# Kernel optimization log

Hardware: AMD Instinct MI355X
Metric: run time of the kernel (lower is better)

Reference implementation:

```python
import jax, jax.numpy as jnp
import numpy as np
from jax import lax

B, H, W, CIN = 4, 64, 64, 1024
CMID = 512
NA = 9  # 3 sizes * 3 ratios
PRE_NMS, POST_NMS, IOU_THR = 6000, 300, 0.7  # eval-mode caps (training=False)


def setup_inputs() -> dict:
    key = jax.random.key(0)
    ks = jax.random.split(key, 4)
    feats = jax.random.normal(ks[0], (B, H, W, CIN), jnp.float32)
    # anchors: normalized ccwh (cx, cy, w, h) on a stride-16 grid of a 1024px image
    stride, img = 16.0, 1024.0
    cx = (jnp.arange(W, dtype=jnp.float32) + 0.5) * stride / img
    cy = (jnp.arange(H, dtype=jnp.float32) + 0.5) * stride / img
    sizes = jnp.array([64.0, 128.0, 256.0])
    ratios = jnp.array([0.5, 1.0, 2.0])
    ws = (sizes[:, None] * jnp.sqrt(ratios)[None, :]).reshape(-1) / img  # [9]
    hs = (sizes[:, None] / jnp.sqrt(ratios)[None, :]).reshape(-1) / img  # [9]
    cyg, cxg = jnp.meshgrid(cy, cx, indexing='ij')  # [H,W]
    ancs = jnp.stack([
        jnp.broadcast_to(cxg[:, :, None], (H, W, NA)),
        jnp.broadcast_to(cyg[:, :, None], (H, W, NA)),
        jnp.broadcast_to(ws[None, None, :], (H, W, NA)),
        jnp.broadcast_to(hs[None, None, :], (H, W, NA)),
    ], axis=-1)
    ancs = jnp.broadcast_to(ancs[None], (B, H, W, NA, 4)).astype(jnp.float32)
    ancs_valid = jnp.ones((B, H, W, NA), jnp.float32)
    w_bneck = jax.random.normal(ks[1], (CIN, CMID), jnp.float32) * 0.01
    b_bneck = jnp.zeros((CMID,), jnp.float32)
    w_cls = jax.random.normal(ks[2], (CMID, NA), jnp.float32) * 0.01
    b_cls = jnp.zeros((NA,), jnp.float32)
    w_reg = jax.random.normal(ks[3], (CMID, NA * 4), jnp.float32) * 0.01
    b_reg = jnp.zeros((NA * 4,), jnp.float32)
    return dict(feats=feats, ancs=ancs, ancs_valid=ancs_valid,
                w_bneck=w_bneck, b_bneck=b_bneck, w_cls=w_cls, b_cls=b_cls,
                w_reg=w_reg, b_reg=b_reg)


def _nms(boxes, max_out, thr):
    # boxes [N,4] xyxy, sorted by score descending. Greedy NMS via lax.scan.
    x1, y1, x2, y2 = boxes[:, 0], boxes[:, 1], boxes[:, 2], boxes[:, 3]
    areas = (x2 - x1) * (y2 - y1)

    def step(valid, _):
        idx = jnp.argmax(valid)  # first still-valid box = highest score
        has = valid[idx]
        b = boxes[idx]
        a = areas[idx]
        iw = jnp.maximum(jnp.minimum(b[2], x2) - jnp.maximum(b[0], x1), 0.0)
        ih = jnp.maximum(jnp.minimum(b[3], y2) - jnp.maximum(b[1], y1), 0.0)
        inter = iw * ih
        union = a + areas - inter
        iou = jnp.where(union > 0, inter / union, 0.0)
        keep = valid & (iou <= thr)
        keep = keep.at[idx].set(False)
        return jnp.where(has, keep, valid), jnp.where(has, idx, -1)

    _, sel = lax.scan(step, jnp.ones(boxes.shape[0], bool), None, length=max_out)
    return sel  # [max_out] selected indices, -1 = no more boxes


def _forward(feats, ancs, w_bneck, b_bneck, w_cls, b_cls, w_reg, b_reg):
    h = jax.nn.relu(jnp.einsum('bhwc,cm->bhwm', feats, w_bneck) + b_bneck)
    cls_pred = jax.nn.sigmoid(jnp.einsum('bhwm,mo->bhwo', h, w_cls) + b_cls)
    reg_pred = (jnp.einsum('bhwm,mo->bhwo', h, w_reg) + b_reg).reshape(B, H, W, NA, 4)
    cls_f = cls_pred.reshape(-1)
    reg_f = reg_pred.reshape(-1, 4)
    anc_f = ancs.reshape(-1, 4)
    # apply_offsets in ccwh: cx += tx*w, cy += ty*h, w *= exp(tw), h *= exp(th)
    cx = anc_f[:, 0] + reg_f[:, 0] * anc_f[:, 2]
    cy = anc_f[:, 1] + reg_f[:, 1] * anc_f[:, 3]
    ww = anc_f[:, 2] * jnp.exp(reg_f[:, 2])
    hh = anc_f[:, 3] * jnp.exp(reg_f[:, 3])
    # ccwh -> xyxy, clip to [0,1]
    boxes = jnp.stack([cx - ww / 2, cy - hh / 2, cx + ww / 2, cy + hh / 2], axis=-1)
    boxes = jnp.clip(boxes, 0.0, 1.0)
    order = jnp.argsort(-cls_f)[:PRE_NMS]
    boxes = boxes[order]
    sel = _nms(boxes, POST_NMS, IOU_THR)
    # pad unselected slots with zeros (TF returns a variable-length tensor)
    proposals = jnp.where(sel[:, None] >= 0, boxes[jnp.clip(sel, 0)], 0.0)
    return cls_pred, reg_pred, proposals


def reference(feats, ancs, ancs_valid, w_bneck, b_bneck, w_cls, b_cls, w_reg, b_reg):
    # ancs_valid is reshaped but never used in the original extract_proposals
    return _forward(feats, ancs, w_bneck, b_bneck, w_cls, b_cls, w_reg, b_reg)
```

## Files before the change

kernel.cpp:

```cpp
#include <hip/hip_runtime.h>
#include <cstdint>
#include <cstddef>

#define P_TOT    16384
#define CIN      1024
#define CMID     512
#define NA       9
#define NANC     147456
#define PRE_NMS  6000
#define POST_NMS 300
#define IOU_THR  0.7f
#define NWORDS   94
#define NHCOPY   64

#define CLS_OFF  0
#define REG_OFF  147456
#define PROP_OFF 737280

#define WS_H        0u
#define WS_MASK     0u
#define WS_HISTN    8388608u
#define WS_LOGITS   33554432u
#define WS_BOXES    36700160u
#define WS_HIST     39059456u
#define WS_WCOMB    39059456u
#define WS_META     39321600u
#define WS_COLL     39321856u
#define WS_SBOX     39387392u
#define CAP_COLL    8192

__device__ __forceinline__ int imin(int a, int b) { return a < b ? a : b; }

__device__ __forceinline__ void gld_lds16(const float* g, float* l) {
    __builtin_amdgcn_global_load_lds(
        (const __attribute__((address_space(1))) void*)g,
        (__attribute__((address_space(3))) void*)l,
        16, 0, 0);
}

__global__ __launch_bounds__(256)
__attribute__((amdgpu_waves_per_eu(1, 2)))
void gemm1_kernel(
    const float* __restrict__ A, const float* __restrict__ Bw,
    const float* __restrict__ bias, float* __restrict__ C)
{
    __shared__ float As[2][16][132];
    __shared__ float Bs[2][16][128];

    const int t  = threadIdx.x;
    const int m0 = blockIdx.x * 128;
    const int n0 = blockIdx.y * 128;
    const int tx = t & 15;
    const int ty = t >> 4;

    const int ar0 = t >> 2;
    const int ac0 = (t & 3) * 4;

    const float* asrc0 = A + (size_t)(m0 + ar0) * CIN + ac0;
    const float* asrc1 = asrc0 + (size_t)64 * CIN;
    const float* bsrc  = Bw + (size_t)(t >> 5) * CMID + n0 + (t & 31) * 4;
    float* bdst0 = &Bs[0][0][0] + t * 4;
    float* bdst1 = &Bs[1][0][0] + t * 4;

    float4 c0a{0,0,0,0}, c0b{0,0,0,0}, c1a{0,0,0,0}, c1b{0,0,0,0};
    float4 c2a{0,0,0,0}, c2b{0,0,0,0}, c3a{0,0,0,0}, c3b{0,0,0,0};
    float4 c4a{0,0,0,0}, c4b{0,0,0,0}, c5a{0,0,0,0}, c5b{0,0,0,0};
    float4 c6a{0,0,0,0}, c6b{0,0,0,0}, c7a{0,0,0,0}, c7b{0,0,0,0};

    gld_lds16(bsrc, bdst0);
    gld_lds16(bsrc + 8 * CMID, bdst0 + 1024);
    float4 pa0 = *(const float4*)(asrc0);
    float4 pa1 = *(const float4*)(asrc1);
    As[0][ac0 + 0][ar0] = pa0.x; As[0][ac0 + 1][ar0] = pa0.y;
    As[0][ac0 + 2][ar0] = pa0.z; As[0][ac0 + 3][ar0] = pa0.w;
    As[0][ac0 + 0][ar0 + 64] = pa1.x; As[0][ac0 + 1][ar0 + 64] = pa1.y;
    As[0][ac0 + 2][ar0 + 64] = pa1.z; As[0][ac0 + 3][ar0 + 64] = pa1.w;
    __syncthreads();

#define FMA4(acc, s, b) { acc.x += (s)*(b).x; acc.y += (s)*(b).y; \
                          acc.z += (s)*(b).z; acc.w += (s)*(b).w; }

    for (int kt = 0; kt < 64; ++kt) {
        const int cur = kt & 1, nxt = cur ^ 1;
        if (kt < 63) {
            const int k0 = (kt + 1) * 16;
            float* bd = nxt ? bdst1 : bdst0;
            gld_lds16(bsrc + (size_t)k0 * CMID, bd);
            gld_lds16(bsrc + (size_t)(k0 + 8) * CMID, bd + 1024);
            pa0 = *(const float4*)(asrc0 + k0);
            pa1 = *(const float4*)(asrc1 + k0);
        }
#pragma unroll 2
        for (int kk = 0; kk < 16; ++kk) {
            float4 a0 = *(const float4*)&As[cur][kk][ty * 4];
            float4 a1 = *(const float4*)&As[cur][kk][64 + ty * 4];
            float4 b0 = *(const float4*)&Bs[cur][kk][tx * 4];
            float4 b1 = *(const float4*)&Bs[cur][kk][64 + tx * 4];
            FMA4(c0a, a0.x, b0) FMA4(c0b, a0.x, b1)
            FMA4(c1a, a0.y, b0) FMA4(c1b, a0.y, b1)
            FMA4(c2a, a0.z, b0) FMA4(c2b, a0.z, b1)
            FMA4(c3a, a0.w, b0) FMA4(c3b, a0.w, b1)
            FMA4(c4a, a1.x, b0) FMA4(c4b, a1.x, b1)
            FMA4(c5a, a1.y, b0) FMA4(c5b, a1.y, b1)
            FMA4(c6a, a1.z, b0) FMA4(c6b, a1.z, b1)
            FMA4(c7a, a1.w, b0) FMA4(c7b, a1.w, b1)
        }
        if (kt < 63) {
            As[nxt][ac0 + 0][ar0] = pa0.x; As[nxt][ac0 + 1][ar0] = pa0.y;
            As[nxt][ac0 + 2][ar0] = pa0.z; As[nxt][ac0 + 3][ar0] = pa0.w;
            As[nxt][ac0 + 0][ar0 + 64] = pa1.x; As[nxt][ac0 + 1][ar0 + 64] = pa1.y;
            As[nxt][ac0 + 2][ar0 + 64] = pa1.z; As[nxt][ac0 + 3][ar0 + 64] = pa1.w;
        }
        __syncthreads();
    }
#undef FMA4

    const float4 bias0 = *(const float4*)(bias + n0 + tx * 4);
    const float4 bias1 = *(const float4*)(bias + n0 + 64 + tx * 4);
#define STROW(row, ca, cb) { \
    float4 o; \
    o.x = fmaxf(ca.x + bias0.x, 0.f); o.y = fmaxf(ca.y + bias0.y, 0.f); \
    o.z = fmaxf(ca.z + bias0.z, 0.f); o.w = fmaxf(ca.w + bias0.w, 0.f); \
    *(float4*)(C + (size_t)(row) * CMID + n0 + tx * 4) = o; \
    o.x = fmaxf(cb.x + bias1.x, 0.f); o.y = fmaxf(cb.y + bias1.y, 0.f); \
    o.z = fmaxf(cb.z + bias1.z, 0.f); o.w = fmaxf(cb.w + bias1.w, 0.f); \
    *(float4*)(C + (size_t)(row) * CMID + n0 + 64 + tx * 4) = o; }

    const int mr = m0 + ty * 4;
    STROW(mr + 0, c0a, c0b)   STROW(mr + 1, c1a, c1b)
    STROW(mr + 2, c2a, c2b)   STROW(mr + 3, c3a, c3b)
    STROW(mr + 64, c4a, c4b)  STROW(mr + 65, c5a, c5b)
    STROW(mr + 66, c6a, c6b)  STROW(mr + 67, c7a, c7b)
#undef STROW
}

__global__ __launch_bounds__(256) void wprep_kernel(
    const float* __restrict__ wcls, const float* __restrict__ wreg,
    float* __restrict__ wcomb)
{
    int i = blockIdx.x * 256 + threadIdx.x;
    int k = i / 48, o = i - k * 48;
    float v = 0.f;
    if (o < 9)       v = wcls[k * 9 + o];
    else if (o < 45) v = wreg[k * 36 + (o - 9)];
    wcomb[i] = v;
}

__global__ __launch_bounds__(256) void gemm2_kernel(
    const float* __restrict__ h, const float* __restrict__ wcomb,
    const float* __restrict__ bcls, const float* __restrict__ breg,
    float* __restrict__ logits)
{
    __shared__ float hS[64][33];
    __shared__ float wS[32][48];

    const int t  = threadIdx.x;
    const int p0 = blockIdx.x * 64;
    const int px = t & 63;
    const int og = t >> 6;

    const int hr = t >> 2;
    const int hc = (t & 3) * 4;

    float acc[12] = {};

    for (int kt = 0; kt < 16; ++kt) {
        const int k0 = kt * 32;
        {
            const float* hp = h + (size_t)(p0 + hr) * CMID + k0 + hc;
            float4 v0 = *(const float4*)(hp);
            float4 v1 = *(const float4*)(hp + 16);
            hS[hr][hc + 0] = v0.x; hS[hr][hc + 1] = v0.y;
            hS[hr][hc + 2] = v0.z; hS[hr][hc + 3] = v0.w;
            hS[hr][16 + hc + 0] = v1.x; hS[hr][16 + hc + 1] = v1.y;
            hS[hr][16 + hc + 2] = v1.z; hS[hr][16 + hc + 3] = v1.w;
        }
        {
            int idx = t;
            if (idx < 384) {
                int kk = idx / 12, o4 = (idx - kk * 12) * 4;
                *(float4*)&wS[kk][o4] = *(const float4*)&wcomb[(size_t)(k0 + kk) * 48 + o4];
            }
            idx = t + 256;
            if (idx < 384) {
                int kk = idx / 12, o4 = (idx - kk * 12) * 4;
                *(float4*)&wS[kk][o4] = *(const float4*)&wcomb[(size_t)(k0 + kk) * 48 + o4];
            }
        }
        __syncthreads();
#pragma unroll 4
        for (int kk = 0; kk < 32; ++kk) {
            float hv = hS[px][kk];
            float4 w0 = *(const float4*)&wS[kk][og * 12];
            float4 w1 = *(const float4*)&wS[kk][og * 12 + 4];
            float4 w2 = *(const float4*)&wS[kk][og * 12 + 8];
            acc[0] += hv * w0.x; acc[1]  += hv * w0.y; acc[2]  += hv * w0.z; acc[3]  += hv * w0.w;
            acc[4] += hv * w1.x; acc[5]  += hv * w1.y; acc[6]  += hv * w1.z; acc[7]  += hv * w1.w;
            acc[8] += hv * w2.x; acc[9]  += hv * w2.y; acc[10] += hv * w2.z; acc[11] += hv * w2.w;
        }
        __syncthreads();
    }
#pragma unroll
    for (int c = 0; c < 12; ++c) {
        int o = og * 12 + c;
        if (o < 45) {
            float bv = (o < 9) ? bcls[o] : breg[o - 9];
            logits[(size_t)(p0 + px) * 48 + o] = acc[c] + bv;
        }
    }
}

__global__ __launch_bounds__(256) void decode_kernel(
    const float* __restrict__ logits, const float4* __restrict__ ancs,
    float* __restrict__ out, float4* __restrict__ boxes,
    unsigned int* __restrict__ histN)
{
    int i = blockIdx.x * 256 + threadIdx.x;
    int p = i / 9, a = i - p * 9;
    const float* lrow = logits + (size_t)p * 48;
    float lg = lrow[a];
    float score = 1.f / (1.f + expf(-lg));
    out[CLS_OFF + i] = score;

    float r0 = lrow[9 + a * 4 + 0];
    float r1 = lrow[9 + a * 4 + 1];
    float r2 = lrow[9 + a * 4 + 2];
    float r3 = lrow[9 + a * 4 + 3];
    float4 rg; rg.x = r0; rg.y = r1; rg.z = r2; rg.w = r3;
    *(float4*)(out + REG_OFF + (size_t)i * 4) = rg;

    float4 an = ancs[i];
    float cx = an.x + r0 * an.z;
    float cy = an.y + r1 * an.w;
    float ww = an.z * expf(r2);
    float hh = an.w * expf(r3);
    float4 bb;
    bb.x = fminf(fmaxf(cx - ww * 0.5f, 0.f), 1.f);
    bb.y = fminf(fmaxf(cy - hh * 0.5f, 0.f), 1.f);
    bb.z = fminf(fmaxf(cx + ww * 0.5f, 0.f), 1.f);
    bb.w = fminf(fmaxf(cy + hh * 0.5f, 0.f), 1.f);
    boxes[i] = bb;

    unsigned int sb = __float_as_uint(score);
    atomicAdd(&histN[(unsigned)(blockIdx.x & (NHCOPY - 1)) * 65536u + (sb >> 16)], 1u);
}

__global__ __launch_bounds__(256) void hreduce_kernel(
    const unsigned int* __restrict__ histN, unsigned int* __restrict__ hist)
{
    int b = blockIdx.x * 256 + threadIdx.x;
    unsigned int s = 0;
#pragma unroll 8
    for (int c = 0; c < NHCOPY; ++c) s += histN[(unsigned)c * 65536u + b];
    hist[b] = s;
}

__global__ __launch_bounds__(256) void scan_kernel(
    const unsigned int* __restrict__ hist, unsigned int* __restrict__ meta)
{
    __shared__ unsigned int sums[256];
    __shared__ unsigned int sc[256];
    __shared__ unsigned int sc2[256];
    __shared__ int cstar;
    __shared__ unsigned int saShared;
    __shared__ int tbin;

    int t = threadIdx.x;
    if (t == 0) tbin = -1;

    unsigned int s = 0;
    int base = t << 8;
    for (int b = 0; b < 256; b += 4) {
        uint4 v = *(const uint4*)(hist + base + b);
        s += v.x + v.y + v.z + v.w;
    }
    sums[t] = s;
    __syncthreads();

    sc[t] = sums[255 - t];
    __syncthreads();
    for (int off = 1; off < 256; off <<= 1) {
        unsigned int v = sc[t];
        unsigned int add = (t >= off) ? sc[t - off] : 0u;
        __syncthreads();
        sc[t] = v + add;
        __syncthreads();
    }
    {
        unsigned int sa = (t == 255) ? 0u : sc[254 - t];
        if (sa < PRE_NMS && sa + sums[t] >= PRE_NMS) { cstar = t; saShared = sa; }
    }
    __syncthreads();

    int c = cstar;
    unsigned int SA = saShared;
    sc2[t] = hist[c * 256 + 255 - t];
    __syncthreads();
    for (int off = 1; off < 256; off <<= 1) {
        unsigned int v = sc2[t];
        unsigned int add = (t >= off) ? sc2[t - off] : 0u;
        __syncthreads();
        sc2[t] = v + add;
        __syncthreads();
    }
    {
        unsigned int si = sc2[255 - t];
        int cand = (SA + si >= PRE_NMS) ? t : -1;
        atomicMax(&tbin, cand);
    }
    __syncthreads();
    if (t == 0) meta[1] = (unsigned int)(c * 256 + tbin);
}

__global__ __launch_bounds__(256) void collect_kernel(
    const float* __restrict__ scores, const unsigned int* __restrict__ meta,
    unsigned long long* __restrict__ coll, unsigned int* __restrict__ cnt)
{
    int i = blockIdx.x * 256 + threadIdx.x;
    unsigned int T = meta[1];
    unsigned int sb = __float_as_uint(scores[i]);
    if ((sb >> 16) >= T) {
        unsigned int pos = atomicAdd(cnt, 1u);
        if (pos < CAP_COLL)
            coll[pos] = ((unsigned long long)sb << 32) |
                        (unsigned long long)(0xFFFFFFFFu - (unsigned int)i);
    }
}

__global__ __launch_bounds__(256) void rank_kernel(
    const unsigned long long* __restrict__ coll,
    const unsigned int* __restrict__ cnt,
    const float4* __restrict__ boxes, float4* __restrict__ sboxes)
{
    const int t = threadIdx.x;
    const int lane = t & 63;
    const int gwave = blockIdx.x * 4 + (t >> 6);
    unsigned int n = cnt[0];
    if (n > CAP_COLL) n = CAP_COLL;
    if (gwave * 16 >= (int)n) return;

    unsigned long long me[16];
    int rank[16];
#pragma unroll
    for (int i = 0; i < 16; ++i) {
        int mi = gwave * 16 + i;
        me[i] = (mi < (int)n) ? coll[mi] : ~0ULL;
        rank[i] = 0;
    }

    for (int j = 0; j < CAP_COLL; j += 64) {
        unsigned long long k = ((unsigned)(j + lane) < n) ? coll[j + lane] : 0ULL;
#pragma unroll
        for (int i = 0; i < 16; ++i)
            rank[i] += (int)__popcll(__ballot(k > me[i]));
    }

#pragma unroll
    for (int i = 0; i < 16; ++i) {
        int mi = gwave * 16 + i;
        if (mi < (int)n && rank[i] < PRE_NMS && lane == i) {
            unsigned int idx = 0xFFFFFFFFu - (unsigned int)(me[i] & 0xFFFFFFFFULL);
            if (idx > NANC - 1) idx = NANC - 1;
            sboxes[rank[i]] = boxes[idx];
        }
    }
}

__global__ __launch_bounds__(64) void nmsmat_kernel(
    const float4* __restrict__ sboxes, unsigned long long* __restrict__ mask)
{
    const int rb = blockIdx.x, cb = blockIdx.y;
    if (cb < rb) return;
    __shared__ float cx1[64], cy1[64], cx2[64], cy2[64], car[64];

    const int t = threadIdx.x;
    const int c = cb * 64 + t;
    float4 b = (c < PRE_NMS) ? sboxes[c] : make_float4(0.f, 0.f, 0.f, 0.f);
    cx1[t] = b.x; cy1[t] = b.y; cx2[t] = b.z; cy2[t] = b.w;
    car[t] = (b.z - b.x) * (b.w - b.y);
    __syncthreads();

    const int r = rb * 64 + t;
    if (r >= PRE_NMS) return;
    const float4 rbx = sboxes[r];
    const float ra = (rbx.z - rbx.x) * (rbx.w - rbx.y);

    unsigned long long w = 0ULL;
#pragma unroll 8
    for (int i = 0; i < 64; ++i) {
        int j = cb * 64 + i;
        float iw = fmaxf(fminf(rbx.z, cx2[i]) - fmaxf(rbx.x, cx1[i]), 0.f);
        float ih = fmaxf(fminf(rbx.w, cy2[i]) - fmaxf(rbx.y, cy1[i]), 0.f);
        float inter = iw * ih;
        float uni = ra + car[i] - inter;
        float iou = (uni > 0.f) ? (inter / uni) : 0.f;
        if (iou > IOU_THR && j > r) w |= (1ULL << i);
    }
    mask[(size_t)r * NWORDS + cb] = w;
}

__global__ __launch_bounds__(64) void nmsresolve_kernel(
    const float4* __restrict__ sboxes,
    const unsigned long long* __restrict__ mask,
    float* __restrict__ prop)
{
    const int t = threadIdx.x;
    for (int j = t; j < POST_NMS * 4; j += 64) prop[j] = 0.f;

    const int w0 = 2 * t, w1 = 2 * t + 1;
    unsigned long long v0 = 0ULL, v1 = 0ULL;
    if (w0 < 93) v0 = ~0ULL; else if (w0 == 93) v0 = (1ULL << 48) - 1ULL;
    if (w1 < 93) v1 = ~0ULL; else if (w1 == 93) v1 = (1ULL << 48) - 1ULL;

    int cnt = 0;
    while (cnt < POST_NMS) {
        int c = 0x7fffffff;
        if (v0) c = (w0 << 6) + __builtin_ctzll(v0);
        else if (v1) c = (w1 << 6) + __builtin_ctzll(v1);
        unsigned long long bal = __ballot((v0 | v1) != 0ULL);
        if (!bal) break;
        int F = __builtin_ctzll(bal);
        int g = __shfl(c, F, 64);
        const int wg = g >> 6, bg = g & 63;

        if (t == 0) {
            float4 bb = sboxes[g];
            *(float4*)(prop + cnt * 4) = bb;
        }
        unsigned long long mx = 0ULL, my = 0ULL;
        if (t < 47) {
            const ulonglong2* row2 = (const ulonglong2*)(mask + (size_t)g * NWORDS);
            ulonglong2 mm = row2[t];
            mx = mm.x; my = mm.y;
        }
        unsigned long long m0 = (w0 >= wg) ? mx : 0ULL;
        unsigned long long m1 = (w1 >= wg) ? my : 0ULL;
        v0 &= ~m0; v1 &= ~m1;
        if (w0 == wg) v0 &= ~(1ULL << bg);
        if (w1 == wg) v1 &= ~(1ULL << bg);
        ++cnt;
    }
}

extern "C" void kernel_launch(void* const* d_in, const int* in_sizes, int n_in,
                              void* d_out, int out_size, void* d_ws, size_t ws_size,
                              hipStream_t stream)
{
    const float*  feats   = (const float*)d_in[0];
    const float4* ancs    = (const float4*)d_in[1];
    const float*  w_bneck = (const float*)d_in[3];
    const float*  b_bneck = (const float*)d_in[4];
    const float*  w_cls   = (const float*)d_in[5];
    const float*  b_cls   = (const float*)d_in[6];
    const float*  w_reg   = (const float*)d_in[7];
    const float*  b_reg   = (const float*)d_in[8];

    float* out = (float*)d_out;
    char*  ws  = (char*)d_ws;
    float*              h      = (float*)(ws + WS_H);
    float*              logits = (float*)(ws + WS_LOGITS);
    float4*             boxes  = (float4*)(ws + WS_BOXES);
    unsigned int*       histN  = (unsigned int*)(ws + WS_HISTN);
    unsigned int*       hist   = (unsigned int*)(ws + WS_HIST);
    float*              wcomb  = (float*)(ws + WS_WCOMB);
    unsigned int*       meta   = (unsigned int*)(ws + WS_META);
    unsigned long long* coll   = (unsigned long long*)(ws + WS_COLL);
    float4*             sboxes = (float4*)(ws + WS_SBOX);
    unsigned long long* mask   = (unsigned long long*)(ws + WS_MASK);

    hipMemsetAsync(ws + WS_META, 0, 256, stream);

    wprep_kernel<<<96, 256, 0, stream>>>(w_cls, w_reg, wcomb);
    gemm1_kernel<<<dim3(128, 4), 256, 0, stream>>>(feats, w_bneck, b_bneck, h);
    gemm2_kernel<<<256, 256, 0, stream>>>(h, wcomb, b_cls, b_reg, logits);
    hipMemsetAsync(ws + WS_HISTN, 0, (size_t)NHCOPY * 65536 * 4, stream);
    decode_kernel<<<576, 256, 0, stream>>>(logits, ancs, out, boxes, histN);
    hreduce_kernel<<<256, 256, 0, stream>>>(histN, hist);
    scan_kernel<<<1, 256, 0, stream>>>(hist, meta);
    collect_kernel<<<576, 256, 0, stream>>>(out, meta, coll, &meta[0]);
    rank_kernel<<<128, 256, 0, stream>>>(coll, meta, boxes, sboxes);
    nmsmat_kernel<<<dim3(94, 94), 64, 0, stream>>>(sboxes, mask);
    nmsresolve_kernel<<<1, 64, 0, stream>>>(sboxes, mask, out + PROP_OFF);
}
```

Baseline: 651.3 us.

## Fuse decode into head GEMM, shrink bottleneck GEMM N-tile, fewer histogram copies

Decode logic (sigmoid, box decoding, histogram atomics) moves into the head GEMM kernel through a shared-memory logits tile, which removes the logits round trip through global memory and one launch. The bottleneck GEMM switches to 128x64 tiles with twice as many blocks and a higher waves-per-EU hint, trading per-block register reuse for occupancy. Histogram replicas drop from 64 to 8, which shrinks the memset and the reduction but raises atomic contention.

```diff
diff --git a/kernel.cpp b/kernel.cpp
--- a/kernel.cpp
+++ b/kernel.cpp
@@ -11,7 +11,7 @@
 #define POST_NMS 300
 #define IOU_THR  0.7f
 #define NWORDS   94
-#define NHCOPY   64
+#define NHCOPY   8
 
 #define CLS_OFF  0
 #define REG_OFF  147456
@@ -19,8 +19,7 @@
 
 #define WS_H        0u
 #define WS_MASK     0u
-#define WS_HISTN    8388608u
-#define WS_LOGITS   33554432u
+#define WS_HISTN    33554432u
 #define WS_BOXES    36700160u
 #define WS_HIST     39059456u
 #define WS_WCOMB    39059456u
@@ -31,7 +30,7 @@
 
 __device__ __forceinline__ int imin(int a, int b) { return a < b ? a : b; }
 
-__device__ __forceinline__ void gld_lds16(const float* g, float* l) {
+__device__ __forceinline__ void gld_lds16f(const float* g, float* l) {
     __builtin_amdgcn_global_load_lds(
         (const __attribute__((address_space(1))) void*)g,
         (__attribute__((address_space(3))) void*)l,
@@ -39,17 +38,17 @@
 }
 
 __global__ __launch_bounds__(256)
-__attribute__((amdgpu_waves_per_eu(1, 2)))
+__attribute__((amdgpu_waves_per_eu(4)))
 void gemm1_kernel(
     const float* __restrict__ A, const float* __restrict__ Bw,
     const float* __restrict__ bias, float* __restrict__ C)
 {
     __shared__ float As[2][16][132];
-    __shared__ float Bs[2][16][128];
+    __shared__ float Bs[2][16][64];
 
     const int t  = threadIdx.x;
     const int m0 = blockIdx.x * 128;
-    const int n0 = blockIdx.y * 128;
+    const int n0 = blockIdx.y * 64;
     const int tx = t & 15;
     const int ty = t >> 4;
 
@@ -58,17 +57,14 @@
 
     const float* asrc0 = A + (size_t)(m0 + ar0) * CIN + ac0;
     const float* asrc1 = asrc0 + (size_t)64 * CIN;
-    const float* bsrc  = Bw + (size_t)(t >> 5) * CMID + n0 + (t & 31) * 4;
+    const float* bsrc  = Bw + (size_t)(t >> 4) * CMID + n0 + (t & 15) * 4;
     float* bdst0 = &Bs[0][0][0] + t * 4;
     float* bdst1 = &Bs[1][0][0] + t * 4;
 
-    float4 c0a{0,0,0,0}, c0b{0,0,0,0}, c1a{0,0,0,0}, c1b{0,0,0,0};
-    float4 c2a{0,0,0,0}, c2b{0,0,0,0}, c3a{0,0,0,0}, c3b{0,0,0,0};
-    float4 c4a{0,0,0,0}, c4b{0,0,0,0}, c5a{0,0,0,0}, c5b{0,0,0,0};
-    float4 c6a{0,0,0,0}, c6b{0,0,0,0}, c7a{0,0,0,0}, c7b{0,0,0,0};
-
-    gld_lds16(bsrc, bdst0);
-    gld_lds16(bsrc + 8 * CMID, bdst0 + 1024);
+    float4 c0{0,0,0,0}, c1{0,0,0,0}, c2{0,0,0,0}, c3{0,0,0,0};
+    float4 c4{0,0,0,0}, c5{0,0,0,0}, c6{0,0,0,0}, c7{0,0,0,0};
+
+    gld_lds16f(bsrc, bdst0);
     float4 pa0 = *(const float4*)(asrc0);
     float4 pa1 = *(const float4*)(asrc1);
     As[0][ac0 + 0][ar0] = pa0.x; As[0][ac0 + 1][ar0] = pa0.y;
@@ -84,9 +80,7 @@
         const int cur = kt & 1, nxt = cur ^ 1;
         if (kt < 63) {
             const int k0 = (kt + 1) * 16;
-            float* bd = nxt ? bdst1 : bdst0;
-            gld_lds16(bsrc + (size_t)k0 * CMID, bd);
-            gld_lds16(bsrc + (size_t)(k0 + 8) * CMID, bd + 1024);
+            gld_lds16f(bsrc + (size_t)k0 * CMID, nxt ? bdst1 : bdst0);
             pa0 = *(const float4*)(asrc0 + k0);
             pa1 = *(const float4*)(asrc1 + k0);
         }
@@ -95,15 +89,14 @@
             float4 a0 = *(const float4*)&As[cur][kk][ty * 4];
             float4 a1 = *(const float4*)&As[cur][kk][64 + ty * 4];
             float4 b0 = *(const float4*)&Bs[cur][kk][tx * 4];
-            float4 b1 = *(const float4*)&Bs[cur][kk][64 + tx * 4];
-            FMA4(c0a, a0.x, b0) FMA4(c0b, a0.x, b1)
-            FMA4(c1a, a0.y, b0) FMA4(c1b, a0.y, b1)
-            FMA4(c2a, a0.z, b0) FMA4(c2b, a0.z, b1)
-            FMA4(c3a, a0.w, b0) FMA4(c3b, a0.w, b1)
-            FMA4(c4a, a1.x, b0) FMA4(c4b, a1.x, b1)
-            FMA4(c5a, a1.y, b0) FMA4(c5b, a1.y, b1)
-            FMA4(c6a, a1.z, b0) FMA4(c6b, a1.z, b1)
-            FMA4(c7a, a1.w, b0) FMA4(c7b, a1.w, b1)
+            FMA4(c0, a0.x, b0)
+            FMA4(c1, a0.y, b0)
+            FMA4(c2, a0.z, b0)
+            FMA4(c3, a0.w, b0)
+            FMA4(c4, a1.x, b0)
+            FMA4(c5, a1.y, b0)
+            FMA4(c6, a1.z, b0)
+            FMA4(c7, a1.w, b0)
         }
         if (kt < 63) {
             As[nxt][ac0 + 0][ar0] = pa0.x; As[nxt][ac0 + 1][ar0] = pa0.y;
@@ -116,21 +109,17 @@
 #undef FMA4
 
     const float4 bias0 = *(const float4*)(bias + n0 + tx * 4);
-    const float4 bias1 = *(const float4*)(bias + n0 + 64 + tx * 4);
-#define STROW(row, ca, cb) { \
+#define STROW(row, ca) { \
     float4 o; \
     o.x = fmaxf(ca.x + bias0.x, 0.f); o.y = fmaxf(ca.y + bias0.y, 0.f); \
     o.z = fmaxf(ca.z + bias0.z, 0.f); o.w = fmaxf(ca.w + bias0.w, 0.f); \
-    *(float4*)(C + (size_t)(row) * CMID + n0 + tx * 4) = o; \
-    o.x = fmaxf(cb.x + bias1.x, 0.f); o.y = fmaxf(cb.y + bias1.y, 0.f); \
-    o.z = fmaxf(cb.z + bias1.z, 0.f); o.w = fmaxf(cb.w + bias1.w, 0.f); \
-    *(float4*)(C + (size_t)(row) * CMID + n0 + 64 + tx * 4) = o; }
+    *(float4*)(C + (size_t)(row) * CMID + n0 + tx * 4) = o; }
 
     const int mr = m0 + ty * 4;
-    STROW(mr + 0, c0a, c0b)   STROW(mr + 1, c1a, c1b)
-    STROW(mr + 2, c2a, c2b)   STROW(mr + 3, c3a, c3b)
-    STROW(mr + 64, c4a, c4b)  STROW(mr + 65, c5a, c5b)
-    STROW(mr + 66, c6a, c6b)  STROW(mr + 67, c7a, c7b)
+    STROW(mr + 0, c0)   STROW(mr + 1, c1)
+    STROW(mr + 2, c2)   STROW(mr + 3, c3)
+    STROW(mr + 64, c4)  STROW(mr + 65, c5)
+    STROW(mr + 66, c6)  STROW(mr + 67, c7)
 #undef STROW
 }
 
@@ -149,10 +138,12 @@
 __global__ __launch_bounds__(256) void gemm2_kernel(
     const float* __restrict__ h, const float* __restrict__ wcomb,
     const float* __restrict__ bcls, const float* __restrict__ breg,
-    float* __restrict__ logits)
+    const float4* __restrict__ ancs, float* __restrict__ out,
+    float4* __restrict__ boxes, unsigned int* __restrict__ histN)
 {
     __shared__ float hS[64][33];
     __shared__ float wS[32][48];
+    __shared__ float lt[64][49];
 
     const int t  = threadIdx.x;
     const int p0 = blockIdx.x * 64;
@@ -200,49 +191,54 @@
         }
         __syncthreads();
     }
+
 #pragma unroll
     for (int c = 0; c < 12; ++c) {
         int o = og * 12 + c;
+        float v = 0.f;
         if (o < 45) {
             float bv = (o < 9) ? bcls[o] : breg[o - 9];
-            logits[(size_t)(p0 + px) * 48 + o] = acc[c] + bv;
-        }
-    }
-}
-
-__global__ __launch_bounds__(256) void decode_kernel(
-    const float* __restrict__ logits, const float4* __restrict__ ancs,
-    float* __restrict__ out, float4* __restrict__ boxes,
-    unsigned int* __restrict__ histN)
-{
-    int i = blockIdx.x * 256 + threadIdx.x;
-    int p = i / 9, a = i - p * 9;
-    const float* lrow = logits + (size_t)p * 48;
-    float lg = lrow[a];
-    float score = 1.f / (1.f + expf(-lg));
-    out[CLS_OFF + i] = score;
-
-    float r0 = lrow[9 + a * 4 + 0];
-    float r1 = lrow[9 + a * 4 + 1];
-    float r2 = lrow[9 + a * 4 + 2];
-    float r3 = lrow[9 + a * 4 + 3];
-    float4 rg; rg.x = r0; rg.y = r1; rg.z = r2; rg.w = r3;
-    *(float4*)(out + REG_OFF + (size_t)i * 4) = rg;
-
-    float4 an = ancs[i];
-    float cx = an.x + r0 * an.z;
-    float cy = an.y + r1 * an.w;
-    float ww = an.z * expf(r2);
-    float hh = an.w * expf(r3);
-    float4 bb;
-    bb.x = fminf(fmaxf(cx - ww * 0.5f, 0.f), 1.f);
-    bb.y = fminf(fmaxf(cy - hh * 0.5f, 0.f), 1.f);
-    bb.z = fminf(fmaxf(cx + ww * 0.5f, 0.f), 1.f);
-    bb.w = fminf(fmaxf(cy + hh * 0.5f, 0.f), 1.f);
-    boxes[i] = bb;
-
-    unsigned int sb = __float_as_uint(score);
-    atomicAdd(&histN[(unsigned)(blockIdx.x & (NHCOPY - 1)) * 65536u + (sb >> 16)], 1u);
+            v = acc[c] + bv;
+        }
+        lt[px][o] = v;
+    }
+    __syncthreads();
+
+#pragma unroll
+    for (int rr = 0; rr < 3; ++rr) {
+        int a_lin = t + rr * 256;
+        if (a_lin < 576) {
+            int px_l = a_lin / 9;
+            int a    = a_lin - px_l * 9;
+            int i    = (p0 + px_l) * 9 + a;
+
+            float lg = lt[px_l][a];
+            float score = 1.f / (1.f + expf(-lg));
+            out[CLS_OFF + i] = score;
+
+            float r0 = lt[px_l][9 + a * 4 + 0];
+            float r1 = lt[px_l][9 + a * 4 + 1];
+            float r2 = lt[px_l][9 + a * 4 + 2];
+            float r3 = lt[px_l][9 + a * 4 + 3];
+            float4 rg; rg.x = r0; rg.y = r1; rg.z = r2; rg.w = r3;
+            *(float4*)(out + REG_OFF + (size_t)i * 4) = rg;
+
+            float4 an = ancs[i];
+            float cx = an.x + r0 * an.z;
+            float cy = an.y + r1 * an.w;
+            float ww = an.z * expf(r2);
+            float hh = an.w * expf(r3);
+            float4 bb;
+            bb.x = fminf(fmaxf(cx - ww * 0.5f, 0.f), 1.f);
+            bb.y = fminf(fmaxf(cy - hh * 0.5f, 0.f), 1.f);
+            bb.z = fminf(fmaxf(cx + ww * 0.5f, 0.f), 1.f);
+            bb.w = fminf(fmaxf(cy + hh * 0.5f, 0.f), 1.f);
+            boxes[i] = bb;
+
+            unsigned int sb = __float_as_uint(score);
+            atomicAdd(&histN[(unsigned)(blockIdx.x & (NHCOPY - 1)) * 65536u + (sb >> 16)], 1u);
+        }
+    }
 }
 
 __global__ __launch_bounds__(256) void hreduce_kernel(
@@ -250,7 +246,7 @@
 {
     int b = blockIdx.x * 256 + threadIdx.x;
     unsigned int s = 0;
-#pragma unroll 8
+#pragma unroll
     for (int c = 0; c < NHCOPY; ++c) s += histN[(unsigned)c * 65536u + b];
     hist[b] = s;
 }
@@ -458,7 +454,6 @@
     float* out = (float*)d_out;
     char*  ws  = (char*)d_ws;
     float*              h      = (float*)(ws + WS_H);
-    float*              logits = (float*)(ws + WS_LOGITS);
     float4*             boxes  = (float4*)(ws + WS_BOXES);
     unsigned int*       histN  = (unsigned int*)(ws + WS_HISTN);
     unsigned int*       hist   = (unsigned int*)(ws + WS_HIST);
@@ -469,12 +464,12 @@
     unsigned long long* mask   = (unsigned long long*)(ws + WS_MASK);
 
     hipMemsetAsync(ws + WS_META, 0, 256, stream);
+    hipMemsetAsync(ws + WS_HISTN, 0, (size_t)NHCOPY * 65536 * 4, stream);
 
     wprep_kernel<<<96, 256, 0, stream>>>(w_cls, w_reg, wcomb);
-    gemm1_kernel<<<dim3(128, 4), 256, 0, stream>>>(feats, w_bneck, b_bneck, h);
-    gemm2_kernel<<<256, 256, 0, stream>>>(h, wcomb, b_cls, b_reg, logits);
-    hipMemsetAsync(ws + WS_HISTN, 0, (size_t)NHCOPY * 65536 * 4, stream);
-    decode_kernel<<<576, 256, 0, stream>>>(logits, ancs, out, boxes, histN);
+    gemm1_kernel<<<dim3(128, 8), 256, 0, stream>>>(feats, w_bneck, b_bneck, h);
+    gemm2_kernel<<<256, 256, 0, stream>>>(h, wcomb, b_cls, b_reg,
+                                          ancs, out, boxes, histN);
     hreduce_kernel<<<256, 256, 0, stream>>>(histN, hist);
     scan_kernel<<<1, 256, 0, stream>>>(hist, meta);
     collect_kernel<<<576, 256, 0, stream>>>(out, meta, coll, &meta[0]);
```

After: 695.7 us. 1.07x slower.

## Fuse decode into head GEMM, deepen GEMM1 K-tile, shrink histogram copies

Applied to the files above, without the earlier changes.

Merges the decode step (sigmoid, box decode, clipping, score histogram) into the 1x1 head GEMM through an LDS logits tile, so the logits round trip through global memory and one launch go away. GEMM2 now uses 32-pixel blocks to get more blocks. GEMM1 loads a 32-deep K tile per stage, which halves the number of barriers but doubles LDS use. Histogram copies drop from 64 to 8, which cuts the memset and reduce traffic but may raise atomic contention.

```diff
diff --git a/kernel.cpp b/kernel.cpp
--- a/kernel.cpp
+++ b/kernel.cpp
@@ -11,7 +11,7 @@
 #define POST_NMS 300
 #define IOU_THR  0.7f
 #define NWORDS   94
-#define NHCOPY   64
+#define NHCOPY   8
 
 #define CLS_OFF  0
 #define REG_OFF  147456
@@ -19,8 +19,7 @@
 
 #define WS_H        0u
 #define WS_MASK     0u
-#define WS_HISTN    8388608u
-#define WS_LOGITS   33554432u
+#define WS_HISTN    33554432u
 #define WS_BOXES    36700160u
 #define WS_HIST     39059456u
 #define WS_WCOMB    39059456u
@@ -31,7 +30,7 @@
 
 __device__ __forceinline__ int imin(int a, int b) { return a < b ? a : b; }
 
-__device__ __forceinline__ void gld_lds16(const float* g, float* l) {
+__device__ __forceinline__ void gld_lds16f(const float* g, float* l) {
     __builtin_amdgcn_global_load_lds(
         (const __attribute__((address_space(1))) void*)g,
         (__attribute__((address_space(3))) void*)l,
@@ -44,8 +43,8 @@
     const float* __restrict__ A, const float* __restrict__ Bw,
     const float* __restrict__ bias, float* __restrict__ C)
 {
-    __shared__ float As[2][16][132];
-    __shared__ float Bs[2][16][128];
+    __shared__ float As[2][32][132];
+    __shared__ float Bs[2][32][128];
 
     const int t  = threadIdx.x;
     const int m0 = blockIdx.x * 128;
@@ -53,45 +52,61 @@
     const int tx = t & 15;
     const int ty = t >> 4;
 
-    const int ar0 = t >> 2;
-    const int ac0 = (t & 3) * 4;
-
-    const float* asrc0 = A + (size_t)(m0 + ar0) * CIN + ac0;
-    const float* asrc1 = asrc0 + (size_t)64 * CIN;
-    const float* bsrc  = Bw + (size_t)(t >> 5) * CMID + n0 + (t & 31) * 4;
-    float* bdst0 = &Bs[0][0][0] + t * 4;
-    float* bdst1 = &Bs[1][0][0] + t * 4;
+    const int ar0 = t >> 1;
+    const int ac0 = (t & 1) * 16;
+
+    const float* asrc = A + (size_t)(m0 + ar0) * CIN + ac0;
+    const float* bsrc = Bw + (size_t)(t >> 5) * CMID + n0 + (t & 31) * 4;
+    float* bflat = &Bs[0][0][0];
 
     float4 c0a{0,0,0,0}, c0b{0,0,0,0}, c1a{0,0,0,0}, c1b{0,0,0,0};
     float4 c2a{0,0,0,0}, c2b{0,0,0,0}, c3a{0,0,0,0}, c3b{0,0,0,0};
     float4 c4a{0,0,0,0}, c4b{0,0,0,0}, c5a{0,0,0,0}, c5b{0,0,0,0};
     float4 c6a{0,0,0,0}, c6b{0,0,0,0}, c7a{0,0,0,0}, c7b{0,0,0,0};
 
-    gld_lds16(bsrc, bdst0);
-    gld_lds16(bsrc + 8 * CMID, bdst0 + 1024);
-    float4 pa0 = *(const float4*)(asrc0);
-    float4 pa1 = *(const float4*)(asrc1);
-    As[0][ac0 + 0][ar0] = pa0.x; As[0][ac0 + 1][ar0] = pa0.y;
-    As[0][ac0 + 2][ar0] = pa0.z; As[0][ac0 + 3][ar0] = pa0.w;
-    As[0][ac0 + 0][ar0 + 64] = pa1.x; As[0][ac0 + 1][ar0 + 64] = pa1.y;
-    As[0][ac0 + 2][ar0 + 64] = pa1.z; As[0][ac0 + 3][ar0 + 64] = pa1.w;
+#define ASTAGE(buf, v0, v1, v2, v3) { \
+    As[buf][ac0 +  0][ar0] = v0.x; As[buf][ac0 +  1][ar0] = v0.y; \
+    As[buf][ac0 +  2][ar0] = v0.z; As[buf][ac0 +  3][ar0] = v0.w; \
+    As[buf][ac0 +  4][ar0] = v1.x; As[buf][ac0 +  5][ar0] = v1.y; \
+    As[buf][ac0 +  6][ar0] = v1.z; As[buf][ac0 +  7][ar0] = v1.w; \
+    As[buf][ac0 +  8][ar0] = v2.x; As[buf][ac0 +  9][ar0] = v2.y; \
+    As[buf][ac0 + 10][ar0] = v2.z; As[buf][ac0 + 11][ar0] = v2.w; \
+    As[buf][ac0 + 12][ar0] = v3.x; As[buf][ac0 + 13][ar0] = v3.y; \
+    As[buf][ac0 + 14][ar0] = v3.z; As[buf][ac0 + 15][ar0] = v3.w; }
+
+    {
+        gld_lds16f(bsrc,                      bflat +    0 + t * 4);
+        gld_lds16f(bsrc + (size_t) 8 * CMID,  bflat + 1024 + t * 4);
+        gld_lds16f(bsrc + (size_t)16 * CMID,  bflat + 2048 + t * 4);
+        gld_lds16f(bsrc + (size_t)24 * CMID,  bflat + 3072 + t * 4);
+        float4 av0 = *(const float4*)(asrc + 0);
+        float4 av1 = *(const float4*)(asrc + 4);
+        float4 av2 = *(const float4*)(asrc + 8);
+        float4 av3 = *(const float4*)(asrc + 12);
+        ASTAGE(0, av0, av1, av2, av3)
+    }
     __syncthreads();
 
 #define FMA4(acc, s, b) { acc.x += (s)*(b).x; acc.y += (s)*(b).y; \
                           acc.z += (s)*(b).z; acc.w += (s)*(b).w; }
 
-    for (int kt = 0; kt < 64; ++kt) {
+    for (int kt = 0; kt < 32; ++kt) {
         const int cur = kt & 1, nxt = cur ^ 1;
-        if (kt < 63) {
-            const int k0 = (kt + 1) * 16;
-            float* bd = nxt ? bdst1 : bdst0;
-            gld_lds16(bsrc + (size_t)k0 * CMID, bd);
-            gld_lds16(bsrc + (size_t)(k0 + 8) * CMID, bd + 1024);
-            pa0 = *(const float4*)(asrc0 + k0);
-            pa1 = *(const float4*)(asrc1 + k0);
+        float4 av0, av1, av2, av3;
+        if (kt < 31) {
+            const int k0 = (kt + 1) * 32;
+            float* bd = bflat + nxt * 4096 + t * 4;
+            gld_lds16f(bsrc + (size_t)(k0     ) * CMID, bd);
+            gld_lds16f(bsrc + (size_t)(k0 +  8) * CMID, bd + 1024);
+            gld_lds16f(bsrc + (size_t)(k0 + 16) * CMID, bd + 2048);
+            gld_lds16f(bsrc + (size_t)(k0 + 24) * CMID, bd + 3072);
+            av0 = *(const float4*)(asrc + k0);
+            av1 = *(const float4*)(asrc + k0 + 4);
+            av2 = *(const float4*)(asrc + k0 + 8);
+            av3 = *(const float4*)(asrc + k0 + 12);
         }
 #pragma unroll 2
-        for (int kk = 0; kk < 16; ++kk) {
+        for (int kk = 0; kk < 32; ++kk) {
             float4 a0 = *(const float4*)&As[cur][kk][ty * 4];
             float4 a1 = *(const float4*)&As[cur][kk][64 + ty * 4];
             float4 b0 = *(const float4*)&Bs[cur][kk][tx * 4];
@@ -105,15 +120,13 @@
             FMA4(c6a, a1.z, b0) FMA4(c6b, a1.z, b1)
             FMA4(c7a, a1.w, b0) FMA4(c7b, a1.w, b1)
         }
-        if (kt < 63) {
-            As[nxt][ac0 + 0][ar0] = pa0.x; As[nxt][ac0 + 1][ar0] = pa0.y;
-            As[nxt][ac0 + 2][ar0] = pa0.z; As[nxt][ac0 + 3][ar0] = pa0.w;
-            As[nxt][ac0 + 0][ar0 + 64] = pa1.x; As[nxt][ac0 + 1][ar0 + 64] = pa1.y;
-            As[nxt][ac0 + 2][ar0 + 64] = pa1.z; As[nxt][ac0 + 3][ar0 + 64] = pa1.w;
+        if (kt < 31) {
+            ASTAGE(nxt, av0, av1, av2, av3)
         }
         __syncthreads();
     }
 #undef FMA4
+#undef ASTAGE
 
     const float4 bias0 = *(const float4*)(bias + n0 + tx * 4);
     const float4 bias1 = *(const float4*)(bias + n0 + 64 + tx * 4);
@@ -149,31 +162,30 @@
 __global__ __launch_bounds__(256) void gemm2_kernel(
     const float* __restrict__ h, const float* __restrict__ wcomb,
     const float* __restrict__ bcls, const float* __restrict__ breg,
-    float* __restrict__ logits)
-{
-    __shared__ float hS[64][33];
+    const float4* __restrict__ ancs, float* __restrict__ out,
+    float4* __restrict__ boxes, unsigned int* __restrict__ histN)
+{
+    __shared__ float hS[32][33];
     __shared__ float wS[32][48];
+    __shared__ float lt[32][49];
 
     const int t  = threadIdx.x;
-    const int p0 = blockIdx.x * 64;
-    const int px = t & 63;
-    const int og = t >> 6;
-
-    const int hr = t >> 2;
-    const int hc = (t & 3) * 4;
-
-    float acc[12] = {};
+    const int p0 = blockIdx.x * 32;
+    const int px = t & 31;
+    const int og = t >> 5;
+
+    const int hr = t >> 3;
+    const int hc = (t & 7) * 4;
+
+    float acc[6] = {};
 
     for (int kt = 0; kt < 16; ++kt) {
         const int k0 = kt * 32;
         {
             const float* hp = h + (size_t)(p0 + hr) * CMID + k0 + hc;
             float4 v0 = *(const float4*)(hp);
-            float4 v1 = *(const float4*)(hp + 16);
             hS[hr][hc + 0] = v0.x; hS[hr][hc + 1] = v0.y;
             hS[hr][hc + 2] = v0.z; hS[hr][hc + 3] = v0.w;
-            hS[hr][16 + hc + 0] = v1.x; hS[hr][16 + hc + 1] = v1.y;
-            hS[hr][16 + hc + 2] = v1.z; hS[hr][16 + hc + 3] = v1.w;
         }
         {
             int idx = t;
@@ -191,58 +203,63 @@
 #pragma unroll 4
         for (int kk = 0; kk < 32; ++kk) {
             float hv = hS[px][kk];
-            float4 w0 = *(const float4*)&wS[kk][og * 12];
-            float4 w1 = *(const float4*)&wS[kk][og * 12 + 4];
-            float4 w2 = *(const float4*)&wS[kk][og * 12 + 8];
-            acc[0] += hv * w0.x; acc[1]  += hv * w0.y; acc[2]  += hv * w0.z; acc[3]  += hv * w0.w;
-            acc[4] += hv * w1.x; acc[5]  += hv * w1.y; acc[6]  += hv * w1.z; acc[7]  += hv * w1.w;
-            acc[8] += hv * w2.x; acc[9]  += hv * w2.y; acc[10] += hv * w2.z; acc[11] += hv * w2.w;
-        }
-        __syncthreads();
-    }
+            float2 w0 = *(const float2*)&wS[kk][og * 6];
+            float2 w1 = *(const float2*)&wS[kk][og * 6 + 2];
+            float2 w2 = *(const float2*)&wS[kk][og * 6 + 4];
+            acc[0] += hv * w0.x; acc[1] += hv * w0.y;
+            acc[2] += hv * w1.x; acc[3] += hv * w1.y;
+            acc[4] += hv * w2.x; acc[5] += hv * w2.y;
+        }
+        __syncthreads();
+    }
+
 #pragma unroll
-    for (int c = 0; c < 12; ++c) {
-        int o = og * 12 + c;
+    for (int c = 0; c < 6; ++c) {
+        int o = og * 6 + c;
+        float v = 0.f;
         if (o < 45) {
             float bv = (o < 9) ? bcls[o] : breg[o - 9];
-            logits[(size_t)(p0 + px) * 48 + o] = acc[c] + bv;
-        }
-    }
-}
-
-__global__ __launch_bounds__(256) void decode_kernel(
-    const float* __restrict__ logits, const float4* __restrict__ ancs,
-    float* __restrict__ out, float4* __restrict__ boxes,
-    unsigned int* __restrict__ histN)
-{
-    int i = blockIdx.x * 256 + threadIdx.x;
-    int p = i / 9, a = i - p * 9;
-    const float* lrow = logits + (size_t)p * 48;
-    float lg = lrow[a];
-    float score = 1.f / (1.f + expf(-lg));
-    out[CLS_OFF + i] = score;
-
-    float r0 = lrow[9 + a * 4 + 0];
-    float r1 = lrow[9 + a * 4 + 1];
-    float r2 = lrow[9 + a * 4 + 2];
-    float r3 = lrow[9 + a * 4 + 3];
-    float4 rg; rg.x = r0; rg.y = r1; rg.z = r2; rg.w = r3;
-    *(float4*)(out + REG_OFF + (size_t)i * 4) = rg;
-
-    float4 an = ancs[i];
-    float cx = an.x + r0 * an.z;
-    float cy = an.y + r1 * an.w;
-    float ww = an.z * expf(r2);
-    float hh = an.w * expf(r3);
-    float4 bb;
-    bb.x = fminf(fmaxf(cx - ww * 0.5f, 0.f), 1.f);
-    bb.y = fminf(fmaxf(cy - hh * 0.5f, 0.f), 1.f);
-    bb.z = fminf(fmaxf(cx + ww * 0.5f, 0.f), 1.f);
-    bb.w = fminf(fmaxf(cy + hh * 0.5f, 0.f), 1.f);
-    boxes[i] = bb;
-
-    unsigned int sb = __float_as_uint(score);
-    atomicAdd(&histN[(unsigned)(blockIdx.x & (NHCOPY - 1)) * 65536u + (sb >> 16)], 1u);
+            v = acc[c] + bv;
+        }
+        lt[px][o] = v;
+    }
+    __syncthreads();
+
+#pragma unroll
+    for (int rr = 0; rr < 2; ++rr) {
+        int a_lin = t + rr * 256;
+        if (a_lin < 288) {
+            int px_l = a_lin / 9;
+            int a    = a_lin - px_l * 9;
+            int i    = (p0 + px_l) * 9 + a;
+
+            float lg = lt[px_l][a];
+            float score = 1.f / (1.f + expf(-lg));
+            out[CLS_OFF + i] = score;
+
+            float r0 = lt[px_l][9 + a * 4 + 0];
+            float r1 = lt[px_l][9 + a * 4 + 1];
+            float r2 = lt[px_l][9 + a * 4 + 2];
+            float r3 = lt[px_l][9 + a * 4 + 3];
+            float4 rg; rg.x = r0; rg.y = r1; rg.z = r2; rg.w = r3;
+            *(float4*)(out + REG_OFF + (size_t)i * 4) = rg;
+
+            float4 an = ancs[i];
+            float cx = an.x + r0 * an.z;
+            float cy = an.y + r1 * an.w;
+            float ww = an.z * expf(r2);
+            float hh = an.w * expf(r3);
+            float4 bb;
+            bb.x = fminf(fmaxf(cx - ww * 0.5f, 0.f), 1.f);
+            bb.y = fminf(fmaxf(cy - hh * 0.5f, 0.f), 1.f);
+            bb.z = fminf(fmaxf(cx + ww * 0.5f, 0.f), 1.f);
+            bb.w = fminf(fmaxf(cy + hh * 0.5f, 0.f), 1.f);
+            boxes[i] = bb;
+
+            unsigned int sb = __float_as_uint(score);
+            atomicAdd(&histN[(unsigned)(blockIdx.x & (NHCOPY - 1)) * 65536u + (sb >> 16)], 1u);
+        }
+    }
 }
 
 __global__ __launch_bounds__(256) void hreduce_kernel(
@@ -250,7 +267,7 @@
 {
     int b = blockIdx.x * 256 + threadIdx.x;
     unsigned int s = 0;
-#pragma unroll 8
+#pragma unroll
     for (int c = 0; c < NHCOPY; ++c) s += histN[(unsigned)c * 65536u + b];
     hist[b] = s;
 }
@@ -458,7 +475,6 @@
     float* out = (float*)d_out;
     char*  ws  = (char*)d_ws;
     float*              h      = (float*)(ws + WS_H);
-    float*              logits = (float*)(ws + WS_LOGITS);
     float4*             boxes  = (float4*)(ws + WS_BOXES);
     unsigned int*       histN  = (unsigned int*)(ws + WS_HISTN);
     unsigned int*       hist   = (unsigned int*)(ws + WS_HIST);
@@ -469,12 +485,12 @@
     unsigned long long* mask   = (unsigned long long*)(ws + WS_MASK);
 
     hipMemsetAsync(ws + WS_META, 0, 256, stream);
+    hipMemsetAsync(ws + WS_HISTN, 0, (size_t)NHCOPY * 65536 * 4, stream);
 
     wprep_kernel<<<96, 256, 0, stream>>>(w_cls, w_reg, wcomb);
     gemm1_kernel<<<dim3(128, 4), 256, 0, stream>>>(feats, w_bneck, b_bneck, h);
-    gemm2_kernel<<<256, 256, 0, stream>>>(h, wcomb, b_cls, b_reg, logits);
-    hipMemsetAsync(ws + WS_HISTN, 0, (size_t)NHCOPY * 65536 * 4, stream);
-    decode_kernel<<<576, 256, 0, stream>>>(logits, ancs, out, boxes, histN);
+    gemm2_kernel<<<512, 256, 0, stream>>>(h, wcomb, b_cls, b_reg,
+                                          ancs, out, boxes, histN);
     hreduce_kernel<<<256, 256, 0, stream>>>(histN, hist);
     scan_kernel<<<1, 256, 0, stream>>>(hist, meta);
     collect_kernel<<<576, 256, 0, stream>>>(out, meta, coll, &meta[0]);
```

Result: no change. 653.8 us (+0.4%).
